# Kernel tuning notes

Hardware: AMD Instinct MI355X
Metric: run time of the kernel (lower is better)

Reference implementation:

```python
import jax, jax.numpy as jnp
import numpy as np

NUM_PHRASES = 24
TOPN = 32
N = NUM_PHRASES * TOPN  # 768 graph nodes (phrase-box candidates)
D = 1024                # visual_dim
NUM_PAIRS = 24          # connected phrase pairs -> E = NUM_PAIRS * TOPN^2 = 24576 edges
STEPS = 1               # cfg.MODEL.RELATION.VISUAL_GRAPH_PASSING_TIME


def _build_graph():
    """Deterministic sparse connectivity: edges between all boxes of connected phrase pairs,
    ordered row-major like np.where(conn_map >= 0) in the original."""
    rng = np.random.default_rng(0)
    pairs = set()
    while len(pairs) < NUM_PAIRS:
        p1, p2 = rng.integers(0, NUM_PHRASES, size=2)
        if p1 != p2:
            pairs.add((int(p1), int(p2)))
    pairs = sorted(pairs)
    sbj_list, obj_list = [], []
    for p1, p2 in pairs:
        s = np.arange(TOPN) + p1 * TOPN
        o = np.arange(TOPN) + p2 * TOPN
        ss, oo = np.meshgrid(s, o, indexing='ij')
        sbj_list.append(ss.ravel())
        obj_list.append(oo.ravel())
    sbj = np.concatenate(sbj_list)
    obj = np.concatenate(obj_list)
    order = np.lexsort((obj, sbj))  # np.where row-major order
    sbj, obj = sbj[order], obj[order]
    involved = np.zeros(N, dtype=bool)
    for p1, p2 in pairs:
        involved[p1 * TOPN:(p1 + 1) * TOPN] = True
        involved[p2 * TOPN:(p2 + 1) * TOPN] = True
    return sbj.astype(np.int32), obj.astype(np.int32), involved


def setup_inputs() -> dict:
    sbj, obj, involved = _build_graph()
    E = sbj.shape[0]
    key = jax.random.key(0)
    ks = jax.random.split(key, 8)
    def w(k, shape, fan_in):
        return jax.random.normal(k, shape, dtype=jnp.float32) / np.float32(np.sqrt(fan_in))
    zD = jnp.zeros((D,), jnp.float32)
    return {
        "visual_feat": jax.random.normal(ks[0], (N, D), jnp.float32),
        "rel_visual_feat": jax.random.normal(ks[1], (E, D), jnp.float32),
        "W_rel": w(ks[2], (3 * D, D), 3 * D), "b_rel": zD,
        "W_sbj": w(ks[3], (2 * D, D), 2 * D), "b_sbj": zD,
        "W_obj": w(ks[4], (2 * D, D), 2 * D), "b_obj": zD,
        "W_ctx": w(ks[5], (D, D), D), "b_ctx": zD,
        "sbj_ind": jnp.asarray(sbj),
        "obj_ind": jnp.asarray(obj),
        "involved_mask": jnp.asarray(involved),
    }


def _edge_softmax(logits, seg, num_segments):
    # masked softmax over the sparse connectivity, normalized per segment (row or column)
    m = jax.ops.segment_max(logits, seg, num_segments=num_segments)
    e = jnp.exp(logits - m[seg])
    s = jax.ops.segment_sum(e, seg, num_segments=num_segments)
    return e / s[seg]


def reference(visual_feat, rel_visual_feat, W_rel, b_rel, W_sbj, b_sbj,
              W_obj, b_obj, W_ctx, b_ctx, sbj_ind, obj_ind, involved_mask):
    n, d = visual_feat.shape
    scale = np.float32(1.0 / np.sqrt(d))
    # split concat-Linear weights so we never materialize [E, 3D]/[E, 2D] concats
    Wr_s, Wr_o, Wr_r = W_rel[:d], W_rel[d:2 * d], W_rel[2 * d:]
    Ws_v, Ws_r = W_sbj[:d], W_sbj[d:]
    Wo_v, Wo_r = W_obj[:d], W_obj[d:]
    vj = visual_feat
    for _ in range(STEPS):
        vs = vj[sbj_ind]          # [E, D] gather
        vo = vj[obj_ind]          # [E, D] gather
        rel = vs @ Wr_s + vo @ Wr_o + rel_visual_feat @ Wr_r + b_rel  # rel_update_embedding
        ts = vs @ Ws_v + rel @ Ws_r + b_sbj   # visual_joint_trans_sbj
        to = vo @ Wo_v + rel @ Wo_r + b_obj   # visual_joint_trans_obj
        logits = jnp.sum(ts * to, axis=1) * scale  # [E]
        w_sbj = _edge_softmax(logits, sbj_ind, n)  # softmax over dim=1 (per subject row)
        w_obj = _edge_softmax(logits, obj_ind, n)  # softmax over dim=0 (per object col)
        # ctx[i] = sum_j w_sbj[i,j] * vj[j] + sum_j w_obj[j,i] * vj[j]  (sparse scatter-add)
        ctx = jax.ops.segment_sum(w_sbj[:, None] * vo, sbj_ind, num_segments=n) \
            + jax.ops.segment_sum(w_obj[:, None] * vs, obj_ind, num_segments=n)
        upd = vj + ctx @ W_ctx + b_ctx  # residual + visual_ctx_embedding, involved nodes only
        vj = jnp.where(involved_mask[:, None], upd, vj)
    return (rel_visual_feat, vj)
```

## Files before the change

### kernel.cpp

```cpp
#include <hip/hip_runtime.h>
#include <hip/hip_bf16.h>
#include <math.h>
#include <type_traits>

typedef __bf16 v8bf __attribute__((ext_vector_type(8)));
typedef __bf16 v4bf __attribute__((ext_vector_type(4)));
typedef float  v4f  __attribute__((ext_vector_type(4)));

__device__ __forceinline__ float wave_reduce_sum(float v) {
#pragma unroll
    for (int m = 1; m < 64; m <<= 1) v += __shfl_xor(v, m, 64);
    return v;
}

__device__ __forceinline__ unsigned fenc(float x) {
    unsigned u = __float_as_uint(x);
    return (u & 0x80000000u) ? ~u : (u | 0x80000000u);
}
__device__ __forceinline__ float fdec(unsigned k) {
    return (k & 0x80000000u) ? __uint_as_float(k ^ 0x80000000u) : __uint_as_float(~k);
}

__device__ __forceinline__ void gload16(const void* g, void* l) {
    __builtin_amdgcn_global_load_lds((const __attribute__((address_space(1))) void*)g,
                                     (__attribute__((address_space(3))) void*)l, 16, 0, 0);
}


__global__ __launch_bounds__(256) void cvt_f32_bf16(const float* __restrict__ in,
                                                    __bf16* __restrict__ out, long long n) {
    long long i = ((long long)blockIdx.x * 256 + threadIdx.x) * 4;
    if (i >= n) return;
    v4f v = *(const v4f*)(in + i);
    v4bf o;
    o[0] = (__bf16)v[0]; o[1] = (__bf16)v[1]; o[2] = (__bf16)v[2]; o[3] = (__bf16)v[3];
    *(v4bf*)(out + i) = o;
}

__global__ __launch_bounds__(256) void megacvt(
    const float* __restrict__ relv, float* __restrict__ outCopy, __bf16* __restrict__ relv_b,
    long long nr,
    const float* __restrict__ wrel, __bf16* __restrict__ wrel_b, long long nw,
    const float* __restrict__ vsrc, __bf16* __restrict__ v_b, long long nv) {
    long long i = ((long long)blockIdx.x * 256 + threadIdx.x) * 4;
    if (i < nr) {
        v4f v = *(const v4f*)(relv + i);
        *(v4f*)(outCopy + i) = v;
        v4bf o;
        o[0] = (__bf16)v[0]; o[1] = (__bf16)v[1]; o[2] = (__bf16)v[2]; o[3] = (__bf16)v[3];
        *(v4bf*)(relv_b + i) = o;
    } else if (i < nr + nw) {
        long long j = i - nr;
        v4f v = *(const v4f*)(wrel + j);
        v4bf o;
        o[0] = (__bf16)v[0]; o[1] = (__bf16)v[1]; o[2] = (__bf16)v[2]; o[3] = (__bf16)v[3];
        *(v4bf*)(wrel_b + j) = o;
    } else if (i < nr + nw + nv) {
        long long j = i - nr - nw;
        v4f v = *(const v4f*)(vsrc + j);
        v4bf o;
        o[0] = (__bf16)v[0]; o[1] = (__bf16)v[1]; o[2] = (__bf16)v[2]; o[3] = (__bf16)v[3];
        *(v4bf*)(v_b + j) = o;
    }
}

__global__ __launch_bounds__(256) void cvt_t_bf16(const float* __restrict__ in,
                                                  __bf16* __restrict__ out, int R, int C) {
    __shared__ float tile[32][33];
    int cb = blockIdx.x * 32, rb = blockIdx.y * 32;
    int tx = threadIdx.x & 31, ty = threadIdx.x >> 5;
#pragma unroll
    for (int i = 0; i < 32; i += 8)
        tile[ty + i][tx] = in[(size_t)(rb + ty + i) * C + cb + tx];
    __syncthreads();
#pragma unroll
    for (int i = 0; i < 32; i += 8)
        out[(size_t)(cb + ty + i) * R + rb + tx] = (__bf16)tile[tx][ty + i];
}

__global__ __launch_bounds__(256) void cvt_t5_bf16(
    const float* __restrict__ in0, __bf16* __restrict__ out0,
    const float* __restrict__ in1, __bf16* __restrict__ out1,
    const float* __restrict__ in2, __bf16* __restrict__ out2,
    const float* __restrict__ in3, __bf16* __restrict__ out3,
    const float* __restrict__ in4, __bf16* __restrict__ out4,
    int Dd, int Nn) {
    __shared__ float tile[32][33];
    const float* in; __bf16* out; int R, C;
    switch (blockIdx.z) {
        case 0: in = in0; out = out0; R = Dd; C = Dd; break;
        case 1: in = in1; out = out1; R = Dd; C = Dd; break;
        case 2: in = in2; out = out2; R = Dd; C = Dd; break;
        case 3: in = in3; out = out3; R = Dd; C = Dd; break;
        default: in = in4; out = out4; R = Nn; C = Dd; break;
    }
    int cb = blockIdx.x * 32, rb = blockIdx.y * 32;
    if (cb >= C || rb >= R) return;
    int tx = threadIdx.x & 31, ty = threadIdx.x >> 5;
#pragma unroll
    for (int i = 0; i < 32; i += 8)
        tile[ty + i][tx] = in[(size_t)(rb + ty + i) * C + cb + tx];
    __syncthreads();
#pragma unroll
    for (int i = 0; i < 32; i += 8)
        out[(size_t)(cb + ty + i) * R + rb + tx] = (__bf16)tile[tx][ty + i];
}

template <int MODE, bool BIG>
__global__ __launch_bounds__(256, 4) void gemm_gl(
    const __bf16* __restrict__ Ap, int ldA,
    const __bf16* __restrict__ Btp, int ldB,
    int M, int N, int K,
    const float* __restrict__ addMat, int ldAdd,
    float* __restrict__ outF,
    __bf16* __restrict__ outB, int ldOut,
    __bf16* __restrict__ outB2,
    const __bf16* __restrict__ rbDot,
    float* __restrict__ qOut,
    const float* __restrict__ addRow,
    const int* __restrict__ maskRow,
    const int* __restrict__ sbjI,
    const int* __restrict__ objI,
    const __bf16* __restrict__ auxW) {
    constexpr int BM = BIG ? 128 : 64;
    constexpr int BN = BIG ? 128 : 64;
    constexpr int WM = BM / 2, WN = BN / 2;
    constexpr int FI = WM / 16, FJ = WN / 16;
    constexpr int NLA = (BM * 64) / 2048;
    constexpr int NLB = (BN * 64) / 2048;

    __shared__ alignas(16) __bf16 As[BM * 64];
    __shared__ alignas(16) __bf16 Bs[BN * 64];

    int m0 = blockIdx.x * BM, n0 = blockIdx.y * BN;
    bool kRows = false;
    if constexpr (MODE == 5) {
        if (m0 >= 2048) {
            kRows = true;
            const __bf16* t = Ap;
            Ap = Btp + (size_t)2 * K * K;
            Btp = t;
            m0 -= 2048;
        }
    }

    const int t = threadIdx.x, lane = t & 63, wid = t >> 6;
    const int wm = wid >> 1, wn = wid & 1;
    const int rA = t >> 3;
    const int cSw = (t & 7) ^ (rA & 7);

    v4f acc[FI][FJ] = {};

    const int l15 = lane & 15;
    const int xorMask = (l15 & 7) << 4;

    for (int kt = 0; kt < K; kt += 64) {
#pragma unroll
        for (int i = 0; i < NLA; ++i)
            gload16(Ap + (size_t)(m0 + i * 32 + rA) * ldA + kt + cSw * 8,
                    (char*)As + i * 4096 + wid * 1024);
#pragma unroll
        for (int i = 0; i < NLB; ++i)
            gload16(Btp + (size_t)(n0 + i * 32 + rA) * ldB + kt + cSw * 8,
                    (char*)Bs + i * 4096 + wid * 1024);
        __syncthreads();
#pragma unroll
        for (int ks = 0; ks < 2; ++ks) {
            const int kb = (ks * 64 + ((lane >> 4) << 4)) ^ xorMask;
            v8bf af[FI], bfr[FJ];
#pragma unroll
            for (int f = 0; f < FI; ++f)
                af[f] = *(const v8bf*)((const char*)As + (wm * WM + f * 16 + l15) * 128 + kb);
#pragma unroll
            for (int f = 0; f < FJ; ++f)
                bfr[f] = *(const v8bf*)((const char*)Bs + (wn * WN + f * 16 + l15) * 128 + kb);
#pragma unroll
            for (int i = 0; i < FI; ++i)
#pragma unroll
                for (int j = 0; j < FJ; ++j)
                    acc[i][j] = __builtin_amdgcn_mfma_f32_16x16x32_bf16(af[i], bfr[j], acc[i][j], 0, 0, 0);
        }
        __syncthreads();
    }

    const int cc = lane & 15, r4 = (lane >> 4) << 2;
    if constexpr (MODE == 3) {
#pragma unroll
        for (int i = 0; i < FI; ++i)
#pragma unroll
            for (int r = 0; r < 4; ++r) {
                const int gm = m0 + wm * WM + i * 16 + r4 + r;
                const int s = sbjI[gm], o = objI[gm];
                const float* Ps = addMat + (size_t)s * ldAdd;
                const float* Qo = outF + (size_t)o * ldAdd;
                float p = 0.f;
#pragma unroll
                for (int j = 0; j < FJ; ++j) {
                    const int gn = n0 + wn * WN + j * 16 + cc;
                    float rv = (float)rbDot[(size_t)gm * N + gn];
                    p += rv * (acc[i][j][r] + Ps[gn] + Qo[gn] + addRow[gn]);
                }
                p += __shfl_xor(p, 1, 64);
                p += __shfl_xor(p, 2, 64);
                p += __shfl_xor(p, 4, 64);
                p += __shfl_xor(p, 8, 64);
                if (cc == 0) atomicAdd(qOut + gm, p);
            }
    } else if constexpr (MODE == 5) {
        if (kRows) {
#pragma unroll
            for (int i = 0; i < FI; ++i)
#pragma unroll
                for (int j = 0; j < FJ; ++j)
#pragma unroll
                    for (int r = 0; r < 4; ++r) {
                        const int gm = m0 + wm * WM + i * 16 + r4 + r;
                        const int gn = n0 + wn * WN + j * 16 + cc;
                        outB2[(size_t)gm * 2048 + gn] = (__bf16)acc[i][j][r];
                    }
        } else {
            const int mb = m0 >> 10, nb = n0 >> 10;
            const int blk = (mb == 0) ? (nb ? 3 : 1) : (nb ? 2 : 0);
            const __bf16* addB = (blk == 0) ? rbDot : (blk == 3 ? auxW : nullptr);
            const size_t DDe = (size_t)ldOut * ldOut;
            __bf16* dst = outB + (size_t)blk * DDe;
#pragma unroll
            for (int i = 0; i < FI; ++i)
#pragma unroll
                for (int j = 0; j < FJ; ++j)
#pragma unroll
                    for (int r = 0; r < 4; ++r) {
                        const int gml = (m0 + wm * WM + i * 16 + r4 + r) & 1023;
                        const int gnl = (n0 + wn * WN + j * 16 + cc) & 1023;
                        float v = acc[i][j][r];
                        if (addB) v += (float)addB[(size_t)gml * ldOut + gnl];
                        dst[(size_t)gml * ldOut + gnl] = (__bf16)v;
                    }
        }
    } else {
#pragma unroll
        for (int i = 0; i < FI; ++i)
#pragma unroll
            for (int j = 0; j < FJ; ++j)
#pragma unroll
                for (int r = 0; r < 4; ++r) {
                    const int gm = m0 + wm * WM + i * 16 + r4 + r;
                    const int gn = n0 + wn * WN + j * 16 + cc;
                    float v = acc[i][j][r];
                    if constexpr (MODE == 0) {
                        if (addMat) v += addMat[(size_t)gm * ldAdd + gn];
                        outB[(size_t)gm * ldOut + gn] = (__bf16)v;
                    } else {
                        float u = addMat[(size_t)gm * ldAdd + gn];
                        if (maskRow[gm]) u += v + addRow[gn];
                        outF[(size_t)gm * ldOut + gn] = u;
                    }
                }
    }
}

__global__ __launch_bounds__(256, 4) void gemm64_pair(
    const __bf16* __restrict__ A0, int ldA0, const __bf16* __restrict__ B0, int ldB0,
    int M0v, int N0v, __bf16* __restrict__ O0, int ldO0,
    const __bf16* __restrict__ A1, int ldA1, const __bf16* __restrict__ B1, int ldB1,
    int M1v, int N1v, __bf16* __restrict__ O1, int ldO1, int K) {
    const __bf16* Ap; const __bf16* Btp; __bf16* Ob;
    int ldA, ldB, Mv, Nv, ldO;
    if (blockIdx.z == 0) { Ap = A0; Btp = B0; Ob = O0; ldA = ldA0; ldB = ldB0; Mv = M0v; Nv = N0v; ldO = ldO0; }
    else                 { Ap = A1; Btp = B1; Ob = O1; ldA = ldA1; ldB = ldB1; Mv = M1v; Nv = N1v; ldO = ldO1; }
    const int m0 = blockIdx.x * 64, n0 = blockIdx.y * 64;
    if (m0 >= Mv || n0 >= Nv) return;

    __shared__ alignas(16) __bf16 As[64 * 64];
    __shared__ alignas(16) __bf16 Bs[64 * 64];
    const int t = threadIdx.x, lane = t & 63, wid = t >> 6;
    const int wm = wid >> 1, wn = wid & 1;
    const int rA = t >> 3;
    const int cSw = (t & 7) ^ (rA & 7);
    const int l15 = lane & 15;
    const int xorMask = (l15 & 7) << 4;
    v4f acc[2][2] = {};

    for (int kt = 0; kt < K; kt += 64) {
#pragma unroll
        for (int i = 0; i < 2; ++i)
            gload16(Ap + (size_t)(m0 + i * 32 + rA) * ldA + kt + cSw * 8,
                    (char*)As + i * 4096 + wid * 1024);
#pragma unroll
        for (int i = 0; i < 2; ++i)
            gload16(Btp + (size_t)(n0 + i * 32 + rA) * ldB + kt + cSw * 8,
                    (char*)Bs + i * 4096 + wid * 1024);
        __syncthreads();
#pragma unroll
        for (int ks = 0; ks < 2; ++ks) {
            const int kb = (ks * 64 + ((lane >> 4) << 4)) ^ xorMask;
            v8bf af[2], bfr[2];
#pragma unroll
            for (int f = 0; f < 2; ++f) {
                af[f]  = *(const v8bf*)((const char*)As + (wm * 32 + f * 16 + l15) * 128 + kb);
                bfr[f] = *(const v8bf*)((const char*)Bs + (wn * 32 + f * 16 + l15) * 128 + kb);
            }
#pragma unroll
            for (int i = 0; i < 2; ++i)
#pragma unroll
                for (int j = 0; j < 2; ++j)
                    acc[i][j] = __builtin_amdgcn_mfma_f32_16x16x32_bf16(af[i], bfr[j], acc[i][j], 0, 0, 0);
        }
        __syncthreads();
    }
    const int cc = lane & 15, r4 = (lane >> 4) << 2;
#pragma unroll
    for (int i = 0; i < 2; ++i)
#pragma unroll
        for (int j = 0; j < 2; ++j)
#pragma unroll
            for (int r = 0; r < 4; ++r) {
                const int gm = m0 + wm * 32 + i * 16 + r4 + r;
                const int gn = n0 + wn * 32 + j * 16 + cc;
                Ob[(size_t)gm * ldO + gn] = (__bf16)acc[i][j][r];
            }
}

__global__ __launch_bounds__(256, 4) void gemm64_quad(
    const __bf16* __restrict__ ACBD, const __bf16* __restrict__ KoKs,
    float* __restrict__ G_AD, float* __restrict__ G_BC,
    float* __restrict__ Pm, float* __restrict__ Qm, int Nn, int Dd) {
    const int z = blockIdx.z;
    const __bf16* Ap = ACBD + (size_t)(z & 1) * 2 * Dd;
    const int ldA = 4 * Dd;
    const __bf16* Btp; int ldB, Nv, K; float* Of; int ldO;
    if (z == 0)      { Btp = ACBD + 3 * Dd; ldB = 4 * Dd; Nv = Nn; K = Dd;     Of = G_AD; ldO = Nn; }
    else if (z == 1) { Btp = ACBD + 1 * Dd; ldB = 4 * Dd; Nv = Nn; K = Dd;     Of = G_BC; ldO = Nn; }
    else             { Btp = KoKs;          ldB = 2 * Dd; Nv = Dd; K = 2 * Dd; Of = (z == 2) ? Pm : Qm; ldO = Dd; }
    const int m0 = blockIdx.x * 64, n0 = blockIdx.y * 64;
    if (n0 >= Nv) return;

    __shared__ alignas(16) __bf16 As[64 * 64];
    __shared__ alignas(16) __bf16 Bs[64 * 64];
    const int t = threadIdx.x, lane = t & 63, wid = t >> 6;
    const int wm = wid >> 1, wn = wid & 1;
    const int rA = t >> 3;
    const int cSw = (t & 7) ^ (rA & 7);
    const int l15 = lane & 15;
    const int xorMask = (l15 & 7) << 4;
    v4f acc[2][2] = {};

    for (int kt = 0; kt < K; kt += 64) {
#pragma unroll
        for (int i = 0; i < 2; ++i)
            gload16(Ap + (size_t)(m0 + i * 32 + rA) * ldA + kt + cSw * 8,
                    (char*)As + i * 4096 + wid * 1024);
#pragma unroll
        for (int i = 0; i < 2; ++i)
            gload16(Btp + (size_t)(n0 + i * 32 + rA) * ldB + kt + cSw * 8,
                    (char*)Bs + i * 4096 + wid * 1024);
        __syncthreads();
#pragma unroll
        for (int ks = 0; ks < 2; ++ks) {
            const int kb = (ks * 64 + ((lane >> 4) << 4)) ^ xorMask;
            v8bf af[2], bfr[2];
#pragma unroll
            for (int f = 0; f < 2; ++f) {
                af[f]  = *(const v8bf*)((const char*)As + (wm * 32 + f * 16 + l15) * 128 + kb);
                bfr[f] = *(const v8bf*)((const char*)Bs + (wn * 32 + f * 16 + l15) * 128 + kb);
            }
#pragma unroll
            for (int i = 0; i < 2; ++i)
#pragma unroll
                for (int j = 0; j < 2; ++j)
                    acc[i][j] = __builtin_amdgcn_mfma_f32_16x16x32_bf16(af[i], bfr[j], acc[i][j], 0, 0, 0);
        }
        __syncthreads();
    }
    const int cc = lane & 15, r4 = (lane >> 4) << 2;
#pragma unroll
    for (int i = 0; i < 2; ++i)
#pragma unroll
        for (int j = 0; j < 2; ++j)
#pragma unroll
            for (int r = 0; r < 4; ++r) {
                const int gm = m0 + wm * 32 + i * 16 + r4 + r;
                const int gn = n0 + wn * 32 + j * 16 + cc;
                Of[(size_t)gm * ldO + gn] = acc[i][j][r];
            }
}


__global__ __launch_bounds__(256) void beta_kernel(
    const float* __restrict__ b_rel, const float* __restrict__ b_sbj, const float* __restrict__ b_obj,
    const float* __restrict__ Wsr, const float* __restrict__ Wor,
    float* __restrict__ bs, float* __restrict__ bo, int D, int rowsPerChunk) {
    const int col = blockIdx.x * 256 + threadIdx.x;
    if (col >= D) return;
    const int r0 = blockIdx.y * rowsPerChunk;
    const float* W = (blockIdx.z == 0) ? Wsr : Wor;
    float acc = 0.f;
    if (blockIdx.y == 0) acc = (blockIdx.z == 0) ? b_sbj[col] : b_obj[col];
    const int rEnd = min(r0 + rowsPerChunk, D);
    for (int r = r0; r < rEnd; ++r)
        acc += b_rel[r] * W[(size_t)r * D + col];
    float* out = (blockIdx.z == 0) ? bs : bo;
    atomicAdd(out + col, acc);
}

__global__ __launch_bounds__(256) void pbeta_kernel(const float* __restrict__ bs,
                                                    const float* __restrict__ bo,
                                                    const __bf16* __restrict__ KoKs,
                                                    float* __restrict__ pb, int D) {
    int d = blockIdx.x * 4 + (threadIdx.x >> 6);
    int lane = threadIdx.x & 63;
    float a = 0.f;
    for (int j = lane; j < D; j += 64)
        a += bs[j] * (float)KoKs[(size_t)d * 2048 + j] + bo[j] * (float)KoKs[(size_t)d * 2048 + 1024 + j];
    a = wave_reduce_sum(a);
    if (lane == 0) pb[d] = a;
}

__global__ __launch_bounds__(256) void node_kernel(
    const __bf16* __restrict__ ACBD,
    const float* __restrict__ bs, const float* __restrict__ bo,
    float* __restrict__ nodeS, float* __restrict__ nodeO, int D) {
    int n = blockIdx.x * 4 + (threadIdx.x >> 6);
    int lane = threadIdx.x & 63;
    int d0 = lane * 16;
    const __bf16* row = ACBD + (size_t)n * 4 * D;
    const __bf16* pa = row + d0;
    const __bf16* pc = row + D + d0;
    const __bf16* pB = row + 2 * D + d0;
    const __bf16* pd = row + 3 * D + d0;
    float s1 = 0.f, s2 = 0.f;
#pragma unroll
    for (int u = 0; u < 16; ++u) {
        float a = (float)pa[u], c = (float)pc[u], b = (float)pB[u], dd = (float)pd[u];
        float vs_ = bs[d0 + u], vo_ = bo[d0 + u];
        s1 += a * c + a * vo_ + vs_ * c;
        s2 += b * dd + b * vo_ + vs_ * dd;
    }
    s1 = wave_reduce_sum(s1);
    s2 = wave_reduce_sum(s2);
    if (lane == 0) { nodeS[n] = s1; nodeO[n] = s2; }
}

__global__ __launch_bounds__(256) void edge_lmax_kernel(
    const float* __restrict__ q,
    const float* __restrict__ nodeS, const float* __restrict__ nodeO,
    const float* __restrict__ G_AD, const float* __restrict__ G_BC,
    const int* __restrict__ sbj, const int* __restrict__ obj,
    float* __restrict__ logits, unsigned* __restrict__ mS, unsigned* __restrict__ mO,
    int E, int Nn, float scale) {
    int e = blockIdx.x * 256 + threadIdx.x;
    if (e >= E) return;
    int s = sbj[e], o = obj[e];
    float l = (q[e] + nodeS[s] + nodeO[o] +
               G_AD[(size_t)s * Nn + o] + G_BC[(size_t)o * Nn + s]) * scale;
    logits[e] = l;
    unsigned k = fenc(l);
    atomicMax(mS + s, k);
    atomicMax(mO + o, k);
}

__global__ __launch_bounds__(256) void expsum_kernel(const float* __restrict__ logits,
                                                     const int* __restrict__ sbj,
                                                     const int* __restrict__ obj,
                                                     const unsigned* __restrict__ mS,
                                                     const unsigned* __restrict__ mO,
                                                     float* __restrict__ es, float* __restrict__ eo,
                                                     float* __restrict__ sumS, float* __restrict__ sumO,
                                                     int E) {
    int e = blockIdx.x * 256 + threadIdx.x;
    if (e >= E) return;
    float l = logits[e];
    int s = sbj[e], o = obj[e];
    float a = expf(l - fdec(mS[s]));
    es[e] = a;
    atomicAdd(sumS + s, a);
    float b = expf(l - fdec(mO[o]));
    eo[e] = b;
    atomicAdd(sumO + o, b);
}

__global__ __launch_bounds__(256) void scatter_kernel(const float* __restrict__ es,
                                                      const float* __restrict__ eo,
                                                      const float* __restrict__ sumS,
                                                      const float* __restrict__ sumO,
                                                      const int* __restrict__ sbj,
                                                      const int* __restrict__ obj,
                                                      float* __restrict__ S, int* __restrict__ inv,
                                                      int E, int Nn) {
    int e = blockIdx.x * 256 + threadIdx.x;
    if (e >= E) return;
    int s = sbj[e], o = obj[e];
    atomicAdd(S + (size_t)s * Nn + o, es[e] / sumS[s]);
    atomicAdd(S + (size_t)o * Nn + s, eo[e] / sumO[o]);
    inv[s] = 1;
    inv[o] = 1;
}


extern "C" void kernel_launch(void* const* d_in, const int* in_sizes, int n_in,
                              void* d_out, int out_size, void* d_ws, size_t ws_size,
                              hipStream_t stream) {
    const float* V     = (const float*)d_in[0];
    const float* relv  = (const float*)d_in[1];
    const float* W_rel = (const float*)d_in[2];
    const float* b_rel = (const float*)d_in[3];
    const float* W_sbj = (const float*)d_in[4];
    const float* b_sbj = (const float*)d_in[5];
    const float* W_obj = (const float*)d_in[6];
    const float* b_obj = (const float*)d_in[7];
    const float* W_ctx = (const float*)d_in[8];
    const float* b_ctx = (const float*)d_in[9];
    const int* sbj = (const int*)d_in[10];
    const int* obj = (const int*)d_in[11];

    const int D  = in_sizes[3];
    const int E  = in_sizes[10];
    const int Nn = in_sizes[12];
    const size_t DD = (size_t)D * D;

    const float* Ws_v = W_sbj;
    const float* Ws_r = W_sbj + DD;
    const float* Wo_v = W_obj;
    const float* Wo_r = W_obj + DD;

    char* ws = (char*)d_ws;
    size_t off = 0;
    auto alloc = [&](size_t bytes) -> void* {
        void* p = (void*)(ws + off);
        off += (bytes + 255) & ~(size_t)255;
        return p;
    };

    __bf16* relv_b = (__bf16*)alloc((size_t)E * D * 2);
    __bf16* Vb     = (__bf16*)alloc((size_t)Nn * D * 2);
    __bf16* VbT    = (__bf16*)alloc((size_t)D * Nn * 2);
    __bf16* ZT_b   = (__bf16*)alloc(DD * 2);
    __bf16* KoKs   = (__bf16*)alloc((size_t)D * 2 * D * 2);
    __bf16* ACBD   = (__bf16*)alloc((size_t)Nn * 4 * D * 2);
    __bf16* Ws_vT  = (__bf16*)alloc(DD * 2);
    __bf16* Wo_vT  = (__bf16*)alloc(DD * 2);
    size_t r1 = off;
    __bf16* Wr_all = (__bf16*)(ws + r1);
    float*  G_AD   = (float*)(ws + r1);
    float*  G_BC   = G_AD + (size_t)Nn * Nn;
    {
        size_t a = 3 * DD * 2, b = 2 * (size_t)Nn * Nn * 4;
        off += ((a > b ? a : b) + 255) & ~(size_t)255;
    }
    size_t r2 = off;
    __bf16* WoWs_T = (__bf16*)(ws + r2);
    __bf16* W_ctxT = (__bf16*)(ws + r2);
    off += 2 * DD * 2;
    size_t r3 = off;
    __bf16* MT_all = (__bf16*)(ws + r3);
    float*  Pm     = (float*)(ws + r3);
    float*  Qm     = Pm + (size_t)Nn * D;
    {
        size_t a = 4 * DD * 2, b = 2 * (size_t)Nn * D * 4;
        off += ((a > b ? a : b) + 255) & ~(size_t)255;
    }
    float* pb     = (float*)alloc((size_t)D * 4);
    float* nodeS  = (float*)alloc((size_t)Nn * 4);
    float* nodeO  = (float*)alloc((size_t)Nn * 4);
    float* logits = (float*)alloc((size_t)E * 4);
    float* es     = (float*)alloc((size_t)E * 4);
    float* eo     = (float*)alloc((size_t)E * 4);
    size_t zbeg = off;
    float* S      = (float*)alloc((size_t)Nn * Nn * 4);
    float* q      = (float*)alloc((size_t)E * 4);
    float* bs     = (float*)alloc((size_t)D * 4);
    float* bo     = (float*)alloc((size_t)D * 4);
    unsigned* mS  = (unsigned*)alloc((size_t)Nn * 4);
    unsigned* mO  = (unsigned*)alloc((size_t)Nn * 4);
    float* sumS   = (float*)alloc((size_t)Nn * 4);
    float* sumO   = (float*)alloc((size_t)Nn * 4);
    int* inv      = (int*)alloc((size_t)Nn * 4);
    size_t zend = off;
    __bf16* Sb    = (__bf16*)alloc((size_t)Nn * Nn * 2);
    __bf16* ctx_b = (__bf16*)alloc((size_t)Nn * D * 2);
    (void)ws_size; (void)n_in; (void)out_size;

    float* outVj = (float*)d_out + (size_t)E * D;

    hipMemsetAsync(ws + zbeg, 0, zend - zbeg, stream);

    {
        long long nr = (long long)E * D, nw = 3 * (long long)DD, nv = (long long)Nn * D;
        long long total = nr + nw + nv;
        int blocks = (int)((total / 4 + 255) / 256);
        megacvt<<<dim3(blocks), dim3(256), 0, stream>>>(
            relv, (float*)d_out, relv_b, nr, W_rel, Wr_all, nw, V, Vb, nv);
    }
    cvt_t5_bf16<<<dim3(D / 32, D / 32, 5), dim3(256), 0, stream>>>(
        Wo_r, WoWs_T, Ws_r, WoWs_T + DD, Ws_v, Ws_vT, Wo_v, Wo_vT, V, VbT, D, Nn);

    beta_kernel<<<dim3((D + 255) / 256, 32, 2), dim3(256), 0, stream>>>(
        b_rel, b_sbj, b_obj, Ws_r, Wo_r, bs, bo, D, (D + 31) / 32);

    gemm_gl<5, true><<<dim3(24, 16), dim3(256), 0, stream>>>(
        WoWs_T, D, Wr_all, D, 3 * D, 2 * D, D, nullptr, 0, nullptr, MT_all, D,
        KoKs, Ws_vT, nullptr, nullptr, nullptr, nullptr, nullptr, Wo_vT);

    cvt_t_bf16<<<dim3(D / 32, D / 32), dim3(256), 0, stream>>>(W_ctx, W_ctxT, D, D);

    gemm64_pair<<<dim3(16, 64, 2), dim3(256), 0, stream>>>(
        KoKs + 0, 2 * D, KoKs + D, 2 * D, D, D, ZT_b, D,
        Vb, D, MT_all, D, Nn, 4 * D, ACBD, 4 * D, D);

    pbeta_kernel<<<dim3(D / 4), dim3(256), 0, stream>>>(bs, bo, KoKs, pb, D);

    gemm64_quad<<<dim3(Nn / 64, 16, 4), dim3(256), 0, stream>>>(
        ACBD, KoKs, G_AD, G_BC, Pm, Qm, Nn, D);

    node_kernel<<<dim3(Nn / 4), dim3(256), 0, stream>>>(ACBD, bs, bo, nodeS, nodeO, D);

    gemm_gl<3, true><<<dim3(E / 128, D / 128), dim3(256), 0, stream>>>(
        relv_b, D, ZT_b, D, E, D, D, Pm, D, Qm, nullptr, 0, nullptr,
        relv_b, q, pb, nullptr, sbj, obj, nullptr);

    edge_lmax_kernel<<<dim3(E / 256), dim3(256), 0, stream>>>(
        q, nodeS, nodeO, G_AD, G_BC, sbj, obj, logits, mS, mO, E, Nn, 1.0f / sqrtf((float)D));
    expsum_kernel<<<dim3(E / 256), dim3(256), 0, stream>>>(logits, sbj, obj, mS, mO, es, eo, sumS, sumO, E);
    scatter_kernel<<<dim3(E / 256), dim3(256), 0, stream>>>(es, eo, sumS, sumO, sbj, obj, S, inv, E, Nn);

    {
        size_t n = (size_t)Nn * Nn;
        cvt_f32_bf16<<<dim3((int)((n / 4 + 255) / 256)), dim3(256), 0, stream>>>(S, Sb, (long long)n);
    }
    gemm_gl<0, false><<<dim3(Nn / 64, D / 64), dim3(256), 0, stream>>>(
        Sb, Nn, VbT, Nn, Nn, D, Nn, nullptr, 0, nullptr, ctx_b, D,
        nullptr, nullptr, nullptr, nullptr, nullptr, nullptr, nullptr, nullptr);
    gemm_gl<4, false><<<dim3(Nn / 64, D / 64), dim3(256), 0, stream>>>(
        ctx_b, D, W_ctxT, D, Nn, D, D, V, D, outVj, nullptr, D,
        nullptr, nullptr, nullptr, b_ctx, inv, nullptr, nullptr, nullptr);
}
```

Before: 333.2 us.

## Fuse small prep kernels into batched launches and enlarge pair GEMM tiles

Folds the bias-projection computation into the megacvt launch as extra blocks, moves the W_ctx transpose into the batched transpose kernel, and merges the pbeta and node reductions into the quad GEMM launch as a fifth z-slice. The pair GEMM moves from 64x64 to 128x128 tiles. W_ctxT gets its own buffer instead of aliasing WoWs_T. Together this removes several kernel launches and the serialization gaps between them. The cost is larger per-block register and LDS use in the GEMM, fewer blocks to spread across CUs, and heterogeneous blocks within one launch.

```diff
diff --git a/kernel.cpp b/kernel.cpp
--- a/kernel.cpp
+++ b/kernel.cpp
@@ -41,8 +41,28 @@
     const float* __restrict__ relv, float* __restrict__ outCopy, __bf16* __restrict__ relv_b,
     long long nr,
     const float* __restrict__ wrel, __bf16* __restrict__ wrel_b, long long nw,
-    const float* __restrict__ vsrc, __bf16* __restrict__ v_b, long long nv) {
-    long long i = ((long long)blockIdx.x * 256 + threadIdx.x) * 4;
+    const float* __restrict__ vsrc, __bf16* __restrict__ v_b, long long nv,
+    long long NB,
+    const float* __restrict__ b_rel, const float* __restrict__ b_sbj, const float* __restrict__ b_obj,
+    const float* __restrict__ Wsr, const float* __restrict__ Wor,
+    float* __restrict__ bs, float* __restrict__ bo, int D) {
+    long long blk = blockIdx.x;
+    if (blk >= NB) {
+        int bb = (int)(blk - NB);
+        const int col = (bb & 3) * 256 + threadIdx.x;
+        const int chunk = (bb >> 2) & 31;
+        const int mat = bb >> 7;
+        const int rpc = D / 32;
+        const int r0 = chunk * rpc;
+        const float* W = (mat == 0) ? Wsr : Wor;
+        float acc = 0.f;
+        if (chunk == 0) acc = (mat == 0) ? b_sbj[col] : b_obj[col];
+        for (int r = r0; r < r0 + rpc; ++r)
+            acc += b_rel[r] * W[(size_t)r * D + col];
+        atomicAdd(((mat == 0) ? bs : bo) + col, acc);
+        return;
+    }
+    long long i = (blk * 256 + threadIdx.x) * 4;
     if (i < nr) {
         v4f v = *(const v4f*)(relv + i);
         *(v4f*)(outCopy + i) = v;
@@ -64,26 +84,13 @@
     }
 }
 
-__global__ __launch_bounds__(256) void cvt_t_bf16(const float* __restrict__ in,
-                                                  __bf16* __restrict__ out, int R, int C) {
-    __shared__ float tile[32][33];
-    int cb = blockIdx.x * 32, rb = blockIdx.y * 32;
-    int tx = threadIdx.x & 31, ty = threadIdx.x >> 5;
-#pragma unroll
-    for (int i = 0; i < 32; i += 8)
-        tile[ty + i][tx] = in[(size_t)(rb + ty + i) * C + cb + tx];
-    __syncthreads();
-#pragma unroll
-    for (int i = 0; i < 32; i += 8)
-        out[(size_t)(cb + ty + i) * R + rb + tx] = (__bf16)tile[tx][ty + i];
-}
-
-__global__ __launch_bounds__(256) void cvt_t5_bf16(
+__global__ __launch_bounds__(256) void cvt_t6_bf16(
     const float* __restrict__ in0, __bf16* __restrict__ out0,
     const float* __restrict__ in1, __bf16* __restrict__ out1,
     const float* __restrict__ in2, __bf16* __restrict__ out2,
     const float* __restrict__ in3, __bf16* __restrict__ out3,
     const float* __restrict__ in4, __bf16* __restrict__ out4,
+    const float* __restrict__ in5, __bf16* __restrict__ out5,
     int Dd, int Nn) {
     __shared__ float tile[32][33];
     const float* in; __bf16* out; int R, C;
@@ -92,7 +99,8 @@
         case 1: in = in1; out = out1; R = Dd; C = Dd; break;
         case 2: in = in2; out = out2; R = Dd; C = Dd; break;
         case 3: in = in3; out = out3; R = Dd; C = Dd; break;
-        default: in = in4; out = out4; R = Nn; C = Dd; break;
+        case 4: in = in4; out = out4; R = Nn; C = Dd; break;
+        default: in = in5; out = out5; R = Dd; C = Dd; break;
     }
     int cb = blockIdx.x * 32, rb = blockIdx.y * 32;
     if (cb >= C || rb >= R) return;
@@ -259,7 +267,7 @@
     }
 }
 
-__global__ __launch_bounds__(256, 4) void gemm64_pair(
+__global__ __launch_bounds__(256, 4) void gemm128_pair(
     const __bf16* __restrict__ A0, int ldA0, const __bf16* __restrict__ B0, int ldB0,
     int M0v, int N0v, __bf16* __restrict__ O0, int ldO0,
     const __bf16* __restrict__ A1, int ldA1, const __bf16* __restrict__ B1, int ldB1,
@@ -268,8 +276,110 @@
     int ldA, ldB, Mv, Nv, ldO;
     if (blockIdx.z == 0) { Ap = A0; Btp = B0; Ob = O0; ldA = ldA0; ldB = ldB0; Mv = M0v; Nv = N0v; ldO = ldO0; }
     else                 { Ap = A1; Btp = B1; Ob = O1; ldA = ldA1; ldB = ldB1; Mv = M1v; Nv = N1v; ldO = ldO1; }
+    const int m0 = blockIdx.x * 128, n0 = blockIdx.y * 128;
+    if (m0 >= Mv || n0 >= Nv) return;
+
+    __shared__ alignas(16) __bf16 As[128 * 64];
+    __shared__ alignas(16) __bf16 Bs[128 * 64];
+    const int t = threadIdx.x, lane = t & 63, wid = t >> 6;
+    const int wm = wid >> 1, wn = wid & 1;
+    const int rA = t >> 3;
+    const int cSw = (t & 7) ^ (rA & 7);
+    const int l15 = lane & 15;
+    const int xorMask = (l15 & 7) << 4;
+    v4f acc[4][4] = {};
+
+    for (int kt = 0; kt < K; kt += 64) {
+#pragma unroll
+        for (int i = 0; i < 4; ++i)
+            gload16(Ap + (size_t)(m0 + i * 32 + rA) * ldA + kt + cSw * 8,
+                    (char*)As + i * 4096 + wid * 1024);
+#pragma unroll
+        for (int i = 0; i < 4; ++i)
+            gload16(Btp + (size_t)(n0 + i * 32 + rA) * ldB + kt + cSw * 8,
+                    (char*)Bs + i * 4096 + wid * 1024);
+        __syncthreads();
+#pragma unroll
+        for (int ks = 0; ks < 2; ++ks) {
+            const int kb = (ks * 64 + ((lane >> 4) << 4)) ^ xorMask;
+            v8bf af[4], bfr[4];
+#pragma unroll
+            for (int f = 0; f < 4; ++f) {
+                af[f]  = *(const v8bf*)((const char*)As + (wm * 64 + f * 16 + l15) * 128 + kb);
+                bfr[f] = *(const v8bf*)((const char*)Bs + (wn * 64 + f * 16 + l15) * 128 + kb);
+            }
+#pragma unroll
+            for (int i = 0; i < 4; ++i)
+#pragma unroll
+                for (int j = 0; j < 4; ++j)
+                    acc[i][j] = __builtin_amdgcn_mfma_f32_16x16x32_bf16(af[i], bfr[j], acc[i][j], 0, 0, 0);
+        }
+        __syncthreads();
+    }
+    const int cc = lane & 15, r4 = (lane >> 4) << 2;
+#pragma unroll
+    for (int i = 0; i < 4; ++i)
+#pragma unroll
+        for (int j = 0; j < 4; ++j)
+#pragma unroll
+            for (int r = 0; r < 4; ++r) {
+                const int gm = m0 + wm * 64 + i * 16 + r4 + r;
+                const int gn = n0 + wn * 64 + j * 16 + cc;
+                Ob[(size_t)gm * ldO + gn] = (__bf16)acc[i][j][r];
+            }
+}
+
+__global__ __launch_bounds__(256, 4) void gemm64_penta(
+    const __bf16* __restrict__ ACBD, const __bf16* __restrict__ KoKs,
+    float* __restrict__ G_AD, float* __restrict__ G_BC,
+    float* __restrict__ Pm, float* __restrict__ Qm,
+    const float* __restrict__ bs, const float* __restrict__ bo,
+    float* __restrict__ pb, float* __restrict__ nodeS, float* __restrict__ nodeO,
+    int Nn, int Dd) {
+    const int z = blockIdx.z;
+    if (z == 4) {
+        const int bb = blockIdx.y * 16 + blockIdx.x;
+        const int w = threadIdx.x >> 6, lane = threadIdx.x & 63;
+        {
+            const int d = bb * 4 + w;
+            float a = 0.f;
+            for (int j = lane; j < Dd; j += 64)
+                a += bs[j] * (float)KoKs[(size_t)d * 2048 + j] +
+                     bo[j] * (float)KoKs[(size_t)d * 2048 + 1024 + j];
+            a = wave_reduce_sum(a);
+            if (lane == 0) pb[d] = a;
+        }
+        if (bb * 4 + w < Nn) {
+            const int n = bb * 4 + w;
+            const int d0 = lane * 16;
+            const __bf16* row = ACBD + (size_t)n * 4 * Dd;
+            const __bf16* pa = row + d0;
+            const __bf16* pc = row + Dd + d0;
+            const __bf16* pB = row + 2 * Dd + d0;
+            const __bf16* pd = row + 3 * Dd + d0;
+            float s1 = 0.f, s2 = 0.f;
+#pragma unroll
+            for (int u = 0; u < 16; ++u) {
+                float a = (float)pa[u], c = (float)pc[u], b = (float)pB[u], dd = (float)pd[u];
+                float vs_ = bs[d0 + u], vo_ = bo[d0 + u];
+                s1 += a * c + a * vo_ + vs_ * c;
+                s2 += b * dd + b * vo_ + vs_ * dd;
+            }
+            s1 = wave_reduce_sum(s1);
+            s2 = wave_reduce_sum(s2);
+            if (lane == 0) { nodeS[n] = s1; nodeO[n] = s2; }
+        }
+        return;
+    }
+
+    const __bf16* Ap = ACBD + (size_t)(z & 1) * 2 * Dd;
+    const int ldA = 4 * Dd;
+    const __bf16* Btp; int ldB, Nv, K; float* Of; int ldO;
+    if (z == 0)      { Btp = ACBD + 3 * Dd; ldB = 4 * Dd; Nv = Nn; K = Dd;     Of = G_AD; ldO = Nn; }
+    else if (z == 1) { Btp = ACBD + 1 * Dd; ldB = 4 * Dd; Nv = Nn; K = Dd;     Of = G_BC; ldO = Nn; }
+    else             { Btp = KoKs;          ldB = 2 * Dd; Nv = Dd; K = 2 * Dd; Of = (z == 2) ? Pm : Qm; ldO = Dd; }
     const int m0 = blockIdx.x * 64, n0 = blockIdx.y * 64;
-    if (m0 >= Mv || n0 >= Nv) return;
+    if (m0 >= Nn || n0 >= Nv) return;
 
     __shared__ alignas(16) __bf16 As[64 * 64];
     __shared__ alignas(16) __bf16 Bs[64 * 64];
@@ -317,129 +427,10 @@
             for (int r = 0; r < 4; ++r) {
                 const int gm = m0 + wm * 32 + i * 16 + r4 + r;
                 const int gn = n0 + wn * 32 + j * 16 + cc;
-                Ob[(size_t)gm * ldO + gn] = (__bf16)acc[i][j][r];
-            }
-}
-
-__global__ __launch_bounds__(256, 4) void gemm64_quad(
-    const __bf16* __restrict__ ACBD, const __bf16* __restrict__ KoKs,
-    float* __restrict__ G_AD, float* __restrict__ G_BC,
-    float* __restrict__ Pm, float* __restrict__ Qm, int Nn, int Dd) {
-    const int z = blockIdx.z;
-    const __bf16* Ap = ACBD + (size_t)(z & 1) * 2 * Dd;
-    const int ldA = 4 * Dd;
-    const __bf16* Btp; int ldB, Nv, K; float* Of; int ldO;
-    if (z == 0)      { Btp = ACBD + 3 * Dd; ldB = 4 * Dd; Nv = Nn; K = Dd;     Of = G_AD; ldO = Nn; }
-    else if (z == 1) { Btp = ACBD + 1 * Dd; ldB = 4 * Dd; Nv = Nn; K = Dd;     Of = G_BC; ldO = Nn; }
-    else             { Btp = KoKs;          ldB = 2 * Dd; Nv = Dd; K = 2 * Dd; Of = (z == 2) ? Pm : Qm; ldO = Dd; }
-    const int m0 = blockIdx.x * 64, n0 = blockIdx.y * 64;
-    if (n0 >= Nv) return;
-
-    __shared__ alignas(16) __bf16 As[64 * 64];
-    __shared__ alignas(16) __bf16 Bs[64 * 64];
-    const int t = threadIdx.x, lane = t & 63, wid = t >> 6;
-    const int wm = wid >> 1, wn = wid & 1;
-    const int rA = t >> 3;
-    const int cSw = (t & 7) ^ (rA & 7);
-    const int l15 = lane & 15;
-    const int xorMask = (l15 & 7) << 4;
-    v4f acc[2][2] = {};
-
-    for (int kt = 0; kt < K; kt += 64) {
-#pragma unroll
-        for (int i = 0; i < 2; ++i)
-            gload16(Ap + (size_t)(m0 + i * 32 + rA) * ldA + kt + cSw * 8,
-                    (char*)As + i * 4096 + wid * 1024);
-#pragma unroll
-        for (int i = 0; i < 2; ++i)
-            gload16(Btp + (size_t)(n0 + i * 32 + rA) * ldB + kt + cSw * 8,
-                    (char*)Bs + i * 4096 + wid * 1024);
-        __syncthreads();
-#pragma unroll
-        for (int ks = 0; ks < 2; ++ks) {
-            const int kb = (ks * 64 + ((lane >> 4) << 4)) ^ xorMask;
-            v8bf af[2], bfr[2];
-#pragma unroll
-            for (int f = 0; f < 2; ++f) {
-                af[f]  = *(const v8bf*)((const char*)As + (wm * 32 + f * 16 + l15) * 128 + kb);
-                bfr[f] = *(const v8bf*)((const char*)Bs + (wn * 32 + f * 16 + l15) * 128 + kb);
-            }
-#pragma unroll
-            for (int i = 0; i < 2; ++i)
-#pragma unroll
-                for (int j = 0; j < 2; ++j)
-                    acc[i][j] = __builtin_amdgcn_mfma_f32_16x16x32_bf16(af[i], bfr[j], acc[i][j], 0, 0, 0);
-        }
-        __syncthreads();
-    }
-    const int cc = lane & 15, r4 = (lane >> 4) << 2;
-#pragma unroll
-    for (int i = 0; i < 2; ++i)
-#pragma unroll
-        for (int j = 0; j < 2; ++j)
-#pragma unroll
-            for (int r = 0; r < 4; ++r) {
-                const int gm = m0 + wm * 32 + i * 16 + r4 + r;
-                const int gn = n0 + wn * 32 + j * 16 + cc;
                 Of[(size_t)gm * ldO + gn] = acc[i][j][r];
             }
 }
 
-
-__global__ __launch_bounds__(256) void beta_kernel(
-    const float* __restrict__ b_rel, const float* __restrict__ b_sbj, const float* __restrict__ b_obj,
-    const float* __restrict__ Wsr, const float* __restrict__ Wor,
-    float* __restrict__ bs, float* __restrict__ bo, int D, int rowsPerChunk) {
-    const int col = blockIdx.x * 256 + threadIdx.x;
-    if (col >= D) return;
-    const int r0 = blockIdx.y * rowsPerChunk;
-    const float* W = (blockIdx.z == 0) ? Wsr : Wor;
-    float acc = 0.f;
-    if (blockIdx.y == 0) acc = (blockIdx.z == 0) ? b_sbj[col] : b_obj[col];
-    const int rEnd = min(r0 + rowsPerChunk, D);
-    for (int r = r0; r < rEnd; ++r)
-        acc += b_rel[r] * W[(size_t)r * D + col];
-    float* out = (blockIdx.z == 0) ? bs : bo;
-    atomicAdd(out + col, acc);
-}
-
-__global__ __launch_bounds__(256) void pbeta_kernel(const float* __restrict__ bs,
-                                                    const float* __restrict__ bo,
-                                                    const __bf16* __restrict__ KoKs,
-                                                    float* __restrict__ pb, int D) {
-    int d = blockIdx.x * 4 + (threadIdx.x >> 6);
-    int lane = threadIdx.x & 63;
-    float a = 0.f;
-    for (int j = lane; j < D; j += 64)
-        a += bs[j] * (float)KoKs[(size_t)d * 2048 + j] + bo[j] * (float)KoKs[(size_t)d * 2048 + 1024 + j];
-    a = wave_reduce_sum(a);
-    if (lane == 0) pb[d] = a;
-}
-
-__global__ __launch_bounds__(256) void node_kernel(
-    const __bf16* __restrict__ ACBD,
-    const float* __restrict__ bs, const float* __restrict__ bo,
-    float* __restrict__ nodeS, float* __restrict__ nodeO, int D) {
-    int n = blockIdx.x * 4 + (threadIdx.x >> 6);
-    int lane = threadIdx.x & 63;
-    int d0 = lane * 16;
-    const __bf16* row = ACBD + (size_t)n * 4 * D;
-    const __bf16* pa = row + d0;
-    const __bf16* pc = row + D + d0;
-    const __bf16* pB = row + 2 * D + d0;
-    const __bf16* pd = row + 3 * D + d0;
-    float s1 = 0.f, s2 = 0.f;
-#pragma unroll
-    for (int u = 0; u < 16; ++u) {
-        float a = (float)pa[u], c = (float)pc[u], b = (float)pB[u], dd = (float)pd[u];
-        float vs_ = bs[d0 + u], vo_ = bo[d0 + u];
-        s1 += a * c + a * vo_ + vs_ * c;
-        s2 += b * dd + b * vo_ + vs_ * dd;
-    }
-    s1 = wave_reduce_sum(s1);
-    s2 = wave_reduce_sum(s2);
-    if (lane == 0) { nodeS[n] = s1; nodeO[n] = s2; }
-}
 
 __global__ __launch_bounds__(256) void edge_lmax_kernel(
     const float* __restrict__ q,
@@ -539,6 +530,7 @@
     __bf16* ACBD   = (__bf16*)alloc((size_t)Nn * 4 * D * 2);
     __bf16* Ws_vT  = (__bf16*)alloc(DD * 2);
     __bf16* Wo_vT  = (__bf16*)alloc(DD * 2);
+    __bf16* W_ctxT = (__bf16*)alloc(DD * 2);
     size_t r1 = off;
     __bf16* Wr_all = (__bf16*)(ws + r1);
     float*  G_AD   = (float*)(ws + r1);
@@ -547,10 +539,7 @@
         size_t a = 3 * DD * 2, b = 2 * (size_t)Nn * Nn * 4;
         off += ((a > b ? a : b) + 255) & ~(size_t)255;
     }
-    size_t r2 = off;
-    __bf16* WoWs_T = (__bf16*)(ws + r2);
-    __bf16* W_ctxT = (__bf16*)(ws + r2);
-    off += 2 * DD * 2;
+    __bf16* WoWs_T = (__bf16*)alloc(2 * DD * 2);
     size_t r3 = off;
     __bf16* MT_all = (__bf16*)(ws + r3);
     float*  Pm     = (float*)(ws + r3);
@@ -586,33 +575,24 @@
 
     {
         long long nr = (long long)E * D, nw = 3 * (long long)DD, nv = (long long)Nn * D;
-        long long total = nr + nw + nv;
-        int blocks = (int)((total / 4 + 255) / 256);
-        megacvt<<<dim3(blocks), dim3(256), 0, stream>>>(
-            relv, (float*)d_out, relv_b, nr, W_rel, Wr_all, nw, V, Vb, nv);
-    }
-    cvt_t5_bf16<<<dim3(D / 32, D / 32, 5), dim3(256), 0, stream>>>(
-        Wo_r, WoWs_T, Ws_r, WoWs_T + DD, Ws_v, Ws_vT, Wo_v, Wo_vT, V, VbT, D, Nn);
-
-    beta_kernel<<<dim3((D + 255) / 256, 32, 2), dim3(256), 0, stream>>>(
-        b_rel, b_sbj, b_obj, Ws_r, Wo_r, bs, bo, D, (D + 31) / 32);
+        long long NB = (nr + nw + nv) / 4 / 256;
+        megacvt<<<dim3((unsigned)(NB + 256)), dim3(256), 0, stream>>>(
+            relv, (float*)d_out, relv_b, nr, W_rel, Wr_all, nw, V, Vb, nv,
+            NB, b_rel, b_sbj, b_obj, Ws_r, Wo_r, bs, bo, D);
+    }
+    cvt_t6_bf16<<<dim3(D / 32, D / 32, 6), dim3(256), 0, stream>>>(
+        Wo_r, WoWs_T, Ws_r, WoWs_T + DD, Ws_v, Ws_vT, Wo_v, Wo_vT, V, VbT, W_ctx, W_ctxT, D, Nn);
 
     gemm_gl<5, true><<<dim3(24, 16), dim3(256), 0, stream>>>(
         WoWs_T, D, Wr_all, D, 3 * D, 2 * D, D, nullptr, 0, nullptr, MT_all, D,
         KoKs, Ws_vT, nullptr, nullptr, nullptr, nullptr, nullptr, Wo_vT);
 
-    cvt_t_bf16<<<dim3(D / 32, D / 32), dim3(256), 0, stream>>>(W_ctx, W_ctxT, D, D);
-
-    gemm64_pair<<<dim3(16, 64, 2), dim3(256), 0, stream>>>(
+    gemm128_pair<<<dim3(8, 32, 2), dim3(256), 0, stream>>>(
         KoKs + 0, 2 * D, KoKs + D, 2 * D, D, D, ZT_b, D,
         Vb, D, MT_all, D, Nn, 4 * D, ACBD, 4 * D, D);
 
-    pbeta_kernel<<<dim3(D / 4), dim3(256), 0, stream>>>(bs, bo, KoKs, pb, D);
-
-    gemm64_quad<<<dim3(Nn / 64, 16, 4), dim3(256), 0, stream>>>(
-        ACBD, KoKs, G_AD, G_BC, Pm, Qm, Nn, D);
-
-    node_kernel<<<dim3(Nn / 4), dim3(256), 0, stream>>>(ACBD, bs, bo, nodeS, nodeO, D);
+    gemm64_penta<<<dim3(16, 16, 5), dim3(256), 0, stream>>>(
+        ACBD, KoKs, G_AD, G_BC, Pm, Qm, bs, bo, pb, nodeS, nodeO, Nn, D);
 
     gemm_gl<3, true><<<dim3(E / 128, D / 128), dim3(256), 0, stream>>>(
         relv_b, D, ZT_b, D, E, D, D, Pm, D, Qm, nullptr, 0, nullptr,
```

New measurement: 330.4 us. About the same (-0.8%).
